# Kernel optimization log

Hardware: AMD Instinct MI355X
Metric: run time of the kernel (lower is better)

Reference implementation:

```python
import jax, jax.numpy as jnp
import numpy as np

B, T, DIM, H, HD = 1, 4096, 1024, 8, 128
ATTN_SCALE = 0.12


def _rms_norm(x):
    # F.rms_norm with default eps = finfo(dtype).eps, no learned weight
    eps = jnp.asarray(jnp.finfo(x.dtype).eps, x.dtype)
    return x * jax.lax.rsqrt(jnp.mean(x * x, axis=-1, keepdims=True) + eps)


def _rotary(x):
    # x: [B, T, H, D]; half-rotary: last D/2 freqs are zero (identity)
    t, d = x.shape[1], x.shape[-1]
    freqs = (1.0 / 1024.0) ** jnp.linspace(0.0, 1.0, d // 4, dtype=jnp.float32)
    freqs = jnp.concatenate([freqs, jnp.zeros(d // 4, dtype=jnp.float32)])
    theta = jnp.arange(t, dtype=jnp.float32)[:, None] * freqs[None, :]  # [T, D/2]
    cos = jnp.cos(theta)[None, :, None, :]
    sin = jnp.sin(theta)[None, :, None, :]
    x1, x2 = jnp.split(x.astype(jnp.float32), 2, axis=-1)
    y = jnp.concatenate([x1 * cos + x2 * sin, -x1 * sin + x2 * cos], axis=-1)
    return y.astype(x.dtype)


def setup_inputs() -> dict:
    key = jax.random.key(0)
    k1, k2, k3, k4, k5 = jax.random.split(key, 5)
    std = 0.5 * DIM ** -0.5
    bound = (3.0 ** 0.5) * std
    x = jax.random.normal(k1, (B, T, DIM), dtype=jnp.float32)
    ve = jax.random.normal(k2, (B, T, DIM), dtype=jnp.float32)
    qkv_w = jax.random.uniform(k3, (3, H * HD, DIM), dtype=jnp.float32,
                               minval=-bound, maxval=bound)
    lambdas = jnp.array([0.5, 0.5], dtype=jnp.float32)
    # c_proj is zero-initialized in the source; use small random weights so the
    # output (and gradients) are non-trivial for correctness testing
    c_proj_w = jax.random.normal(k4, (DIM, H * HD), dtype=jnp.float32) * 0.02
    docs = jnp.sort(jax.random.randint(k5, (T,), 0, 8, dtype=jnp.int32))
    return {"x": x, "ve": ve, "qkv_w": qkv_w, "lambdas": lambdas,
            "c_proj_w": c_proj_w, "docs": docs}


def reference(x, ve, qkv_w, lambdas, c_proj_w, docs):
    b, t, _ = x.shape
    w = qkv_w.reshape(3 * H * HD, -1)              # [3*hdim, dim]
    qkv = (x @ w.T).reshape(b, t, 3, H, HD)        # chunk(3, dim=-2) == axis 2 here
    q, k, v = qkv[:, :, 0], qkv[:, :, 1], qkv[:, :, 2]
    q, k = _rms_norm(q), _rms_norm(k)
    q, k = _rotary(q), _rotary(k)
    v = lambdas[0] * v + lambdas[1] * ve.reshape(v.shape)
    # doc-causal mask: attend within the same document, causally
    i = jnp.arange(t)
    mask = (i[:, None] >= i[None, :]) & (docs[:, None] == docs[None, :])  # [T, T]
    scores = jnp.einsum('bihd,bjhd->bhij', q, k) * ATTN_SCALE
    scores = jnp.where(mask[None, None], scores, -jnp.inf)
    p = jax.nn.softmax(scores, axis=-1)
    y = jnp.einsum('bhij,bjhd->bihd', p, v).reshape(b, t, H * HD)
    return y @ c_proj_w.T
```

## Files before the change

### kernel.cpp

```cpp
#include <hip/hip_runtime.h>
#include <hip/hip_bf16.h>
#include <cstdint>

typedef __attribute__((ext_vector_type(8))) short sh8;
typedef __attribute__((ext_vector_type(4))) float f4;
typedef __attribute__((ext_vector_type(16))) float f16v;

#define T_SEQ 4096
#define DIMN  1024
#define NH    8
#define HDIM  128
#define NQKV  3072
#define ATTN_SCALE 0.12f

__device__ __forceinline__ ushort f2bf(float x) {
  __hip_bfloat16 b = __float2bfloat16(x);
  return *reinterpret_cast<ushort*>(&b);
}
__device__ __forceinline__ float bf2f(ushort u) {
  uint v = ((uint)u) << 16;
  float f;
  __builtin_memcpy(&f, &v, 4);
  return f;
}

#define GLDS16(g, l) \
  __builtin_amdgcn_global_load_lds((const __attribute__((address_space(1))) void*)(g), \
                                   (__attribute__((address_space(3))) void*)(l), 16, 0, 0)

template <int N>
__device__ __forceinline__ void wait_vmcnt() {
  if constexpr (N == 0)      asm volatile("s_waitcnt vmcnt(0)" ::: "memory");
  else if constexpr (N == 4) asm volatile("s_waitcnt vmcnt(4)" ::: "memory");
  else if constexpr (N == 6) asm volatile("s_waitcnt vmcnt(6)" ::: "memory");
  else if constexpr (N == 8) asm volatile("s_waitcnt vmcnt(8)" ::: "memory");
  __builtin_amdgcn_sched_barrier(0);
}
#define BAR __builtin_amdgcn_s_barrier()

__global__ __launch_bounds__(256) void k_prep(const float* __restrict__ x,
                                              const float* __restrict__ qw,
                                              const float* __restrict__ cw,
                                              ushort* __restrict__ xb, ushort* __restrict__ wb,
                                              ushort* __restrict__ cbuf,
                                              const int* __restrict__ docs, int* __restrict__ dstart) {
  const int b = blockIdx.x;
  if (b < 8192) {
    const int i = b * 256 + threadIdx.x;
    const float* src;
    ushort* dst;
    int j;
    if (i < 1048576)       { src = x;  dst = xb;   j = i; }
    else if (i < 1835008)  { src = qw; dst = wb;   j = i - 1048576; }
    else                   { src = cw; dst = cbuf; j = i - 1835008; }
    float4 v = reinterpret_cast<const float4*>(src)[j];
    ushort4 o;
    o.x = f2bf(v.x); o.y = f2bf(v.y); o.z = f2bf(v.z); o.w = f2bf(v.w);
    reinterpret_cast<ushort4*>(dst)[j] = o;
  } else {
    const int i = (b - 8192) * 256 + threadIdx.x;
    if (i < T_SEQ) {
      int d = docs[i];
      int lo = 0, hi = i;
      while (lo < hi) { int mid = (lo + hi) >> 1; if (docs[mid] < d) lo = mid + 1; else hi = mid; }
      dstart[i] = lo;
    }
  }
}

__global__ __launch_bounds__(512, 2) void k_gemm32(const ushort* __restrict__ A,
                                                   const ushort* __restrict__ B,
                                                   ushort* __restrict__ C,
                                                   int N, int K) {
  __shared__ ushort lds[2][512 * 64];
  const int tid = threadIdx.x;
  const int lane = tid & 63;
  const int w = tid >> 6;
  const int l5 = lane >> 5;
  const int lr32 = lane & 31;
  const int wave_m = w >> 2, wave_n = w & 3;

  const int bid = blockIdx.x;
  const int s = (bid & 7) * 32 + (bid >> 3);
  const int m0 = ((s >> 5) * 4 + ((s >> 3) & 3)) * 128;
  const int n0 = (s & 7) * 384;

  f16v acc[2][3];
#pragma unroll
  for (int i = 0; i < 2; ++i)
#pragma unroll
    for (int j = 0; j < 3; ++j)
#pragma unroll
      for (int r = 0; r < 16; ++r) acc[i][j][r] = 0.f;

  const int NT = K >> 6;

  auto STAGE4 = [&](int buf, int t, int ug) {
    const int k0 = t << 6;
#pragma unroll
    for (int uu = 0; uu < 4; ++uu) {
      const int u = ug * 4 + uu;
      const int row = u * 64 + (tid >> 3);
      const int c = (tid & 7) ^ (row & 7);
      const ushort* src = (u < 2) ? (A + (size_t)(m0 + row) * K + k0 + c * 8)
                                  : (B + (size_t)(n0 + row - 128) * K + k0 + c * 8);
      GLDS16(src, (char*)&lds[buf][0] + u * 8192 + w * 1024);
    }
  };

  STAGE4(0, 0, 0); STAGE4(0, 0, 1);
  wait_vmcnt<0>();
  BAR;

  int cur = 0;
  for (int t = 0; t < NT; ++t) {
    const bool more = (t + 1) < NT;
    const char* bb = (const char*)&lds[cur][0];

#define RD_FRAGS(ks, a, b)                                                        \
    _Pragma("unroll") for (int mt = 0; mt < 2; ++mt) {                            \
      const int row = wave_m * 64 + mt * 32 + lr32;                               \
      a[mt] = *(const sh8*)(bb + row * 128 + ((((ks) * 2 + l5) ^ (row & 7)) * 16));\
    }                                                                             \
    _Pragma("unroll") for (int nt = 0; nt < 3; ++nt) {                            \
      const int row = 128 + wave_n * 96 + nt * 32 + lr32;                         \
      b[nt] = *(const sh8*)(bb + row * 128 + ((((ks) * 2 + l5) ^ (row & 7)) * 16));\
    }

#define MFMA6(a, b)                                                               \
    __builtin_amdgcn_s_setprio(1);                                                \
    _Pragma("unroll") for (int mt = 0; mt < 2; ++mt)                              \
    _Pragma("unroll") for (int nt = 0; nt < 3; ++nt)                              \
      acc[mt][nt] = __builtin_amdgcn_mfma_f32_32x32x16_bf16(a[mt], b[nt],         \
                                                            acc[mt][nt], 0, 0, 0);\
    __builtin_amdgcn_s_setprio(0);

    {
      sh8 a[2], b[3];
      RD_FRAGS(0, a, b)
      if (more) STAGE4(cur ^ 1, t + 1, 0);
      MFMA6(a, b)
    }
    {
      sh8 a[2], b[3];
      RD_FRAGS(1, a, b)
      if (more) STAGE4(cur ^ 1, t + 1, 1);
      MFMA6(a, b)
    }
    BAR;
    {
      sh8 a[2], b[3];
      RD_FRAGS(2, a, b)
      MFMA6(a, b)
    }
    if (more) wait_vmcnt<4>();
    {
      sh8 a[2], b[3];
      RD_FRAGS(3, a, b)
      MFMA6(a, b)
    }
    if (more) wait_vmcnt<0>();
    BAR;
    cur ^= 1;
  }
#undef RD_FRAGS
#undef MFMA6

#pragma unroll
  for (int mt = 0; mt < 2; ++mt)
#pragma unroll
    for (int nt = 0; nt < 3; ++nt) {
      const int gcol = n0 + wave_n * 96 + nt * 32 + lr32;
#pragma unroll
      for (int r = 0; r < 16; ++r) {
        const int grow = m0 + wave_m * 64 + mt * 32 + (r & 3) + 8 * (r >> 2) + 4 * l5;
        C[(size_t)grow * N + gcol] = f2bf(acc[mt][nt][r]);
      }
    }
}

__global__ __launch_bounds__(256) void k_gemm2(const ushort* __restrict__ A,
                                               const ushort* __restrict__ B,
                                               float* __restrict__ C,
                                               int N, int K, int gx) {
  constexpr int BM = 128, BN = 128;
  constexpr int CHA = BM * 4;
  constexpr int CHT = (BM + BN) * 4;
  constexpr int LPW = CHT / 256;
  constexpr int TILEB = (BM + BN) * 64;

  __shared__ __attribute__((aligned(16))) char lds[3 * TILEB];

  const int tid = threadIdx.x;
  const int lane = tid & 63;
  const int w = tid >> 6;
  const int l5 = lane >> 5;
  const int lr32 = lane & 31;
  const int wm = w >> 1, wn = w & 1;

  const int nwg = gridDim.x;
  const int nb = (blockIdx.x & 7) * (nwg >> 3) + (blockIdx.x >> 3);
  const int m0 = (nb / gx) * BM;
  const int n0 = (nb % gx) * BN;

  f16v acc[2][2];
#pragma unroll
  for (int i = 0; i < 2; ++i)
#pragma unroll
    for (int j = 0; j < 2; ++j)
#pragma unroll
      for (int r = 0; r < 16; ++r) acc[i][j][r] = 0.f;

  const int NT = K >> 5;

  auto STAGE = [&](int t, int buf) {
    const int k0 = t << 5;
#pragma unroll
    for (int l = 0; l < LPW; ++l) {
      const int cb = (l * 4 + w) * 64;
      const int ch = cb + lane;
      const ushort* src;
      if (ch < CHA) {
        const int row = ch >> 2;
        const int cs = (ch & 3) ^ ((row >> 1) & 3);
        src = A + (size_t)(m0 + row) * K + k0 + cs * 8;
      } else {
        const int c2 = ch - CHA;
        const int row = c2 >> 2;
        const int cs = (c2 & 3) ^ ((row >> 1) & 3);
        src = B + (size_t)(n0 + row) * K + k0 + cs * 8;
      }
      GLDS16(src, lds + buf * TILEB + cb * 16);
    }
  };

  STAGE(0, 0);
  STAGE(1, 1);
  wait_vmcnt<LPW>();
  BAR;

  int bufc = 0;
  for (int t = 0; t < NT; ++t) {
    const bool more = (t + 2) < NT;
    if (more) STAGE(t + 2, bufc == 0 ? 2 : (bufc == 1 ? 0 : 1));

    const char* bb = lds + bufc * TILEB;
#pragma unroll
    for (int ks = 0; ks < 2; ++ks) {
      sh8 a[2], b[2];
#pragma unroll
      for (int mt = 0; mt < 2; ++mt) {
        const int row = wm * 64 + mt * 32 + lr32;
        a[mt] = *(const sh8*)(bb + row * 64 + (((ks * 2 + l5) ^ ((row >> 1) & 3)) * 16));
      }
#pragma unroll
      for (int nt = 0; nt < 2; ++nt) {
        const int row = wn * 64 + nt * 32 + lr32;
        b[nt] = *(const sh8*)(bb + BM * 64 + row * 64 + (((ks * 2 + l5) ^ ((row >> 1) & 3)) * 16));
      }
      __builtin_amdgcn_s_setprio(1);
#pragma unroll
      for (int mt = 0; mt < 2; ++mt)
#pragma unroll
        for (int nt = 0; nt < 2; ++nt)
          acc[mt][nt] = __builtin_amdgcn_mfma_f32_32x32x16_bf16(a[mt], b[nt], acc[mt][nt], 0, 0, 0);
      __builtin_amdgcn_s_setprio(0);
    }

    if (more) wait_vmcnt<LPW>();
    else      wait_vmcnt<0>();
    BAR;
    bufc = bufc == 2 ? 0 : bufc + 1;
  }

#pragma unroll
  for (int mt = 0; mt < 2; ++mt)
#pragma unroll
    for (int nt = 0; nt < 2; ++nt) {
      const int gcol = n0 + wn * 64 + nt * 32 + lr32;
#pragma unroll
      for (int r = 0; r < 16; ++r) {
        const int grow = m0 + wm * 64 + mt * 32 + (r & 3) + 8 * (r >> 2) + 4 * l5;
        C[(size_t)grow * N + gcol] = acc[mt][nt][r];
      }
    }
}

__global__ __launch_bounds__(256) void k_fuse(const ushort* __restrict__ qkvb,
                                              const float* __restrict__ ve,
                                              const float* __restrict__ lam,
                                              ushort* __restrict__ qh, ushort* __restrict__ kh,
                                              ushort* __restrict__ vh) {
  const int pair = blockIdx.x * 4 + (threadIdx.x >> 6);
  const int t = pair >> 3, h = pair & 7;
  const int l = threadIdx.x & 63;
  const ushort* base = qkvb + (size_t)t * NQKV + h * HDIM + 2 * l;
  uint qu = *reinterpret_cast<const uint*>(base);
  uint ku = *reinterpret_cast<const uint*>(base + 1024);
  uint vu = *reinterpret_cast<const uint*>(base + 2048);
  float q0 = bf2f((ushort)qu), q1 = bf2f((ushort)(qu >> 16));
  float k0 = bf2f((ushort)ku), k1 = bf2f((ushort)(ku >> 16));
  float v0 = bf2f((ushort)vu), v1 = bf2f((ushort)(vu >> 16));
  float sq = q0 * q0 + q1 * q1, sk = k0 * k0 + k1 * k1;
#pragma unroll
  for (int m = 1; m < 64; m <<= 1) { sq += __shfl_xor(sq, m); sk += __shfl_xor(sk, m); }
  const float eps = 1.1920928955078125e-07f;
  float rq = rsqrtf(sq * (1.f / 128.f) + eps);
  float rk = rsqrtf(sk * (1.f / 128.f) + eps);
  q0 *= rq; q1 *= rq; k0 *= rk; k1 *= rk;
  float c0 = 1.f, s0 = 0.f, c1 = 1.f, s1 = 0.f;
  if ((l & 31) < 16) {
    const int f0 = 2 * (l & 31);
    float fr0 = exp2f(-10.f * (float)f0 * (1.f / 31.f));
    float fr1 = exp2f(-10.f * (float)(f0 + 1) * (1.f / 31.f));
    sincosf((float)t * fr0, &s0, &c0);
    sincosf((float)t * fr1, &s1, &c1);
  }
  float qx0 = __shfl_xor(q0, 32), qx1 = __shfl_xor(q1, 32);
  float kx0 = __shfl_xor(k0, 32), kx1 = __shfl_xor(k1, 32);
  const float sgn = (l < 32) ? 1.f : -1.f;
  float qr0 = q0 * c0 + sgn * qx0 * s0;
  float qr1 = q1 * c1 + sgn * qx1 * s1;
  float kr0 = k0 * c0 + sgn * kx0 * s0;
  float kr1 = k1 * c1 + sgn * kx1 * s1;
  const float l0 = lam[0], l1 = lam[1];
  float2 vev = *reinterpret_cast<const float2*>(ve + (size_t)t * DIMN + h * HDIM + 2 * l);
  float vr0 = l0 * v0 + l1 * vev.x;
  float vr1 = l0 * v1 + l1 * vev.y;
  const size_t o = ((size_t)h * T_SEQ + t) * HDIM + 2 * l;
  *reinterpret_cast<uint*>(qh + o) = (uint)f2bf(qr0) | ((uint)f2bf(qr1) << 16);
  *reinterpret_cast<uint*>(kh + o) = (uint)f2bf(kr0) | ((uint)f2bf(kr1) << 16);
  *reinterpret_cast<uint*>(vh + o) = (uint)f2bf(vr0) | ((uint)f2bf(vr1) << 16);
}

__global__ __launch_bounds__(256) void k_vt(const ushort* __restrict__ vh, ushort* __restrict__ vt) {
  const int tb = blockIdx.x, db = blockIdx.y, h = blockIdx.z;
  __shared__ ushort L[64][68];
  const int tid = threadIdx.x;
  const int t0 = tb * 64, d0 = db * 64;
  const size_t ib = ((size_t)h * T_SEQ + t0) * HDIM + d0;
#pragma unroll
  for (int p = 0; p < 4; ++p) {
    const int row = p * 16 + (tid >> 4);
    const int c4 = (tid & 15) * 4;
    ushort4 v = *reinterpret_cast<const ushort4*>(vh + ib + (size_t)row * HDIM + c4);
    *reinterpret_cast<ushort4*>(&L[row][c4]) = v;
  }
  __syncthreads();
  const size_t ob = ((size_t)h * HDIM + d0) * T_SEQ + t0;
#pragma unroll
  for (int p = 0; p < 4; ++p) {
    const int drow = p * 16 + (tid >> 4);
    const int t4 = (tid & 15) * 4;
    ushort4 v;
    v.x = L[t4 + 0][drow]; v.y = L[t4 + 1][drow];
    v.z = L[t4 + 2][drow]; v.w = L[t4 + 3][drow];
    *reinterpret_cast<ushort4*>(vt + ob + (size_t)drow * T_SEQ + t4) = v;
  }
}

__global__ __launch_bounds__(256) void k_attn(const ushort* __restrict__ qh,
                                              const ushort* __restrict__ kh,
                                              const ushort* __restrict__ vt,
                                              const int* __restrict__ doc_start,
                                              ushort* __restrict__ y) {
  const int h  = blockIdx.x;
  const int qb = blockIdx.y;
  const int q0 = qb * 64;
  const int tid  = threadIdx.x;
  const int wave = tid >> 6;
  const int lane = tid & 63;
  const int lr = lane & 15, lg = lane >> 4;

  __shared__ ushort Ks[2][64 * 128];
  __shared__ ushort Vs[2][128 * 64];
  __shared__ ushort Ps[4][16 * 64];

  const ushort* Kg = kh + (size_t)h * T_SEQ * HDIM;
  const ushort* Vg = vt + (size_t)h * HDIM * T_SEQ;

  const int i_me = q0 + wave * 16 + lr;
  sh8 qf[4];
  {
    const ushort* qp = qh + ((size_t)h * T_SEQ + i_me) * HDIM + lg * 8;
#pragma unroll
    for (int c = 0; c < 4; ++c) qf[c] = *reinterpret_cast<const sh8*>(qp + c * 32);
  }
  const int ds_me = doc_start[i_me];
  const int ds_hi = doc_start[q0 + 63];
  const int kb0   = doc_start[q0] >> 6;

  const f4 fzero = {0.f, 0.f, 0.f, 0.f};
  f4 o_acc[8];
#pragma unroll
  for (int i = 0; i < 8; ++i) o_acc[i] = fzero;
  float m_me = -1e30f, l_me = 0.f;

  auto STAGE = [&](int b, int k0) {
#pragma unroll
    for (int p = 0; p < 4; ++p) {
      const int c = p * 256 + tid;
      const int row = c >> 4, cc = c & 15;
      GLDS16(Kg + (size_t)(k0 + row) * HDIM + (cc ^ (row & 7)) * 8,
             &Ks[b][(p * 256 + wave * 64) * 8]);
    }
#pragma unroll
    for (int p = 0; p < 4; ++p) {
      const int c = p * 256 + tid;
      const int d = c >> 3, cc = c & 7;
      GLDS16(Vg + (size_t)d * T_SEQ + k0 + (cc ^ (d & 7)) * 8,
             &Vs[b][(p * 256 + wave * 64) * 8]);
    }
  };

  int cur = 0;
  STAGE(0, kb0 * 64);

  const int sw = (lr & 7) << 4;

  for (int kb = kb0; kb <= qb; ++kb) {
    const int k0 = kb * 64;
    __syncthreads();
    if (kb < qb) STAGE(cur ^ 1, k0 + 64);

    const char* Kb = (const char*)&Ks[cur][0];
    const char* Vb = (const char*)&Vs[cur][0];
    char* Pw = (char*)&Ps[wave][0];

    f4 sacc[4];
#pragma unroll
    for (int jt = 0; jt < 4; ++jt) sacc[jt] = fzero;
#pragma unroll
    for (int jt = 0; jt < 4; ++jt)
#pragma unroll
      for (int c = 0; c < 4; ++c) {
        sh8 kf = *reinterpret_cast<const sh8*>(Kb + (jt * 16 + lr) * 256 + ((c * 64 + lg * 16) ^ sw));
        sacc[jt] = __builtin_amdgcn_mfma_f32_16x16x32_bf16(kf, qf[c], sacc[jt], 0, 0, 0);
      }

    const bool fullblk = (kb < qb) && (ds_hi <= k0);
    float p[4][4];
#pragma unroll
    for (int jt = 0; jt < 4; ++jt)
#pragma unroll
      for (int r = 0; r < 4; ++r) {
        float s = sacc[jt][r] * ATTN_SCALE;
        const int j = k0 + jt * 16 + lg * 4 + r;
        bool valid = fullblk || ((j <= i_me) && (j >= ds_me));
        p[jt][r] = valid ? s : -1e30f;
      }
    float tm = -1e30f;
#pragma unroll
    for (int jt = 0; jt < 4; ++jt) {
      float a = fmaxf(p[jt][0], p[jt][1]), b = fmaxf(p[jt][2], p[jt][3]);
      tm = fmaxf(tm, fmaxf(a, b));
    }
    tm = fmaxf(tm, __shfl_xor(tm, 16));
    tm = fmaxf(tm, __shfl_xor(tm, 32));
    const float mnew = fmaxf(m_me, tm);
    const float sc = __expf(m_me - mnew);
    m_me = mnew;
    float rs = 0.f;
#pragma unroll
    for (int jt = 0; jt < 4; ++jt)
#pragma unroll
      for (int r = 0; r < 4; ++r) {
        float pv = __expf(p[jt][r] - mnew);
        p[jt][r] = pv;
        rs += pv;
      }
    rs += __shfl_xor(rs, 16);
    rs += __shfl_xor(rs, 32);
    l_me = l_me * sc + rs;

#pragma unroll
    for (int jt = 0; jt < 4; ++jt) {
      uint2 u;
      u.x = (uint)f2bf(p[jt][0]) | ((uint)f2bf(p[jt][1]) << 16);
      u.y = (uint)f2bf(p[jt][2]) | ((uint)f2bf(p[jt][3]) << 16);
      *reinterpret_cast<uint2*>(Pw + lr * 128 + ((jt * 32 + lg * 8) ^ sw)) = u;
    }

    float sco[4];
#pragma unroll
    for (int rr = 0; rr < 4; ++rr) sco[rr] = __shfl(sc, lg * 4 + rr);
#pragma unroll
    for (int dt = 0; dt < 8; ++dt)
#pragma unroll
      for (int rr = 0; rr < 4; ++rr) o_acc[dt][rr] *= sco[rr];

#pragma unroll
    for (int ks = 0; ks < 2; ++ks) {
      sh8 pa = *reinterpret_cast<const sh8*>(Pw + lr * 128 + ((ks * 64 + lg * 16) ^ sw));
#pragma unroll
      for (int dt = 0; dt < 8; ++dt) {
        sh8 vf = *reinterpret_cast<const sh8*>(Vb + (dt * 16 + lr) * 128 + ((ks * 64 + lg * 16) ^ sw));
        o_acc[dt] = __builtin_amdgcn_mfma_f32_16x16x32_bf16(pa, vf, o_acc[dt], 0, 0, 0);
      }
    }

    __builtin_amdgcn_s_barrier();
    cur ^= 1;
  }

  float lo[4];
#pragma unroll
  for (int rr = 0; rr < 4; ++rr) lo[rr] = __shfl(l_me, lg * 4 + rr);
#pragma unroll
  for (int dt = 0; dt < 8; ++dt)
#pragma unroll
    for (int rr = 0; rr < 4; ++rr) {
      const int trow = q0 + wave * 16 + lg * 4 + rr;
      y[(size_t)trow * DIMN + h * HDIM + dt * 16 + lr] = f2bf(o_acc[dt][rr] / lo[rr]);
    }
}

extern "C" void kernel_launch(void* const* d_in, const int* in_sizes, int n_in,
                              void* d_out, int out_size, void* d_ws, size_t ws_size,
                              hipStream_t stream) {
  const float* x    = (const float*)d_in[0];
  const float* ve   = (const float*)d_in[1];
  const float* qkvw = (const float*)d_in[2];
  const float* lam  = (const float*)d_in[3];
  const float* cpw  = (const float*)d_in[4];
  const int*   docs = (const int*)d_in[5];
  float* out = (float*)d_out;
  char* ws = (char*)d_ws;

  ushort* qkvb = (ushort*)(ws);
  ushort* xb   = (ushort*)(ws + (24ull << 20));
  ushort* wb   = (ushort*)(ws + (32ull << 20));
  ushort* cb   = (ushort*)(ws + (38ull << 20));
  ushort* qh   = (ushort*)(ws + (40ull << 20));
  ushort* kh   = (ushort*)(ws + (48ull << 20));
  ushort* vh   = (ushort*)(ws + (56ull << 20));
  ushort* vt   = (ushort*)(ws + (64ull << 20));
  ushort* yb   = (ushort*)(ws + (72ull << 20));
  int*  dstart = (int*)(ws + (80ull << 20));

  k_prep<<<8192 + 16, 256, 0, stream>>>(x, qkvw, cpw, xb, wb, cb, docs, dstart);

  k_gemm32<<<256, 512, 0, stream>>>(xb, wb, qkvb, NQKV, DIMN);

  k_fuse<<<T_SEQ * NH / 4, 256, 0, stream>>>(qkvb, ve, lam, qh, kh, vh);
  k_vt<<<dim3(T_SEQ / 64, HDIM / 64, NH), 256, 0, stream>>>(vh, vt);

  k_attn<<<dim3(NH, T_SEQ / 64), 256, 0, stream>>>(qh, kh, vt, dstart, yb);

  k_gemm2<<<256, 256, 0, stream>>>(yb, cb, out, DIMN, DIMN, DIMN / 128);
}
```

Before: 102.5 us.

## Fuse V transpose into QKV epilogue kernel and retile QKV GEMM to 256x256

Merges the norm/rotary/value-mix kernel with the separate V transpose kernel. V is staged in shared memory and written directly in transposed layout, which removes the intermediate vh buffer round trip and one launch. The QKV GEMM moves from 128x384 tiles on 256 blocks to 256x256 tiles on 192 blocks, with 4x2 MFMA fragments per wave and a mid-iteration vmcnt wait removed. Output stores in both GEMMs become nontemporal. The new GEMM grid leaves some CUs idle, and the fused kernel processes 16 tokens per wave sequentially, which may reduce parallelism.

```diff
diff --git a/kernel.cpp b/kernel.cpp
--- a/kernel.cpp
+++ b/kernel.cpp
@@ -32,7 +32,6 @@
 __device__ __forceinline__ void wait_vmcnt() {
   if constexpr (N == 0)      asm volatile("s_waitcnt vmcnt(0)" ::: "memory");
   else if constexpr (N == 4) asm volatile("s_waitcnt vmcnt(4)" ::: "memory");
-  else if constexpr (N == 6) asm volatile("s_waitcnt vmcnt(6)" ::: "memory");
   else if constexpr (N == 8) asm volatile("s_waitcnt vmcnt(8)" ::: "memory");
   __builtin_amdgcn_sched_barrier(0);
 }
@@ -68,10 +67,10 @@
   }
 }
 
-__global__ __launch_bounds__(512, 2) void k_gemm32(const ushort* __restrict__ A,
-                                                   const ushort* __restrict__ B,
-                                                   ushort* __restrict__ C,
-                                                   int N, int K) {
+__global__ __launch_bounds__(512, 2) void k_gemm256(const ushort* __restrict__ A,
+                                                    const ushort* __restrict__ B,
+                                                    ushort* __restrict__ C,
+                                                    int N, int K) {
   __shared__ ushort lds[2][512 * 64];
   const int tid = threadIdx.x;
   const int lane = tid & 63;
@@ -80,16 +79,15 @@
   const int lr32 = lane & 31;
   const int wave_m = w >> 2, wave_n = w & 3;
 
-  const int bid = blockIdx.x;
-  const int s = (bid & 7) * 32 + (bid >> 3);
-  const int m0 = ((s >> 5) * 4 + ((s >> 3) & 3)) * 128;
-  const int n0 = (s & 7) * 384;
-
-  f16v acc[2][3];
-#pragma unroll
-  for (int i = 0; i < 2; ++i)
-#pragma unroll
-    for (int j = 0; j < 3; ++j)
+  const int nb = (blockIdx.x & 7) * 24 + (blockIdx.x >> 3);
+  const int m0 = (nb / 12) * 256;
+  const int n0 = (nb % 12) * 256;
+
+  f16v acc[4][2];
+#pragma unroll
+  for (int i = 0; i < 4; ++i)
+#pragma unroll
+    for (int j = 0; j < 2; ++j)
 #pragma unroll
       for (int r = 0; r < 16; ++r) acc[i][j][r] = 0.f;
 
@@ -102,8 +100,8 @@
       const int u = ug * 4 + uu;
       const int row = u * 64 + (tid >> 3);
       const int c = (tid & 7) ^ (row & 7);
-      const ushort* src = (u < 2) ? (A + (size_t)(m0 + row) * K + k0 + c * 8)
-                                  : (B + (size_t)(n0 + row - 128) * K + k0 + c * 8);
+      const ushort* src = (row < 256 ? A + (size_t)(m0 + row) * K
+                                     : B + (size_t)(n0 + row - 256) * K) + k0 + c * 8;
       GLDS16(src, (char*)&lds[buf][0] + u * 8192 + w * 1024);
     }
   };
@@ -117,64 +115,63 @@
     const bool more = (t + 1) < NT;
     const char* bb = (const char*)&lds[cur][0];
 
-#define RD_FRAGS(ks, a, b)                                                        \
-    _Pragma("unroll") for (int mt = 0; mt < 2; ++mt) {                            \
-      const int row = wave_m * 64 + mt * 32 + lr32;                               \
+#define RD6(ks, a, b)                                                              \
+    _Pragma("unroll") for (int mt = 0; mt < 4; ++mt) {                             \
+      const int row = wave_m * 128 + mt * 32 + lr32;                               \
       a[mt] = *(const sh8*)(bb + row * 128 + ((((ks) * 2 + l5) ^ (row & 7)) * 16));\
-    }                                                                             \
-    _Pragma("unroll") for (int nt = 0; nt < 3; ++nt) {                            \
-      const int row = 128 + wave_n * 96 + nt * 32 + lr32;                         \
+    }                                                                              \
+    _Pragma("unroll") for (int nt = 0; nt < 2; ++nt) {                             \
+      const int row = 256 + wave_n * 64 + nt * 32 + lr32;                          \
       b[nt] = *(const sh8*)(bb + row * 128 + ((((ks) * 2 + l5) ^ (row & 7)) * 16));\
     }
 
-#define MFMA6(a, b)                                                               \
-    __builtin_amdgcn_s_setprio(1);                                                \
-    _Pragma("unroll") for (int mt = 0; mt < 2; ++mt)                              \
-    _Pragma("unroll") for (int nt = 0; nt < 3; ++nt)                              \
-      acc[mt][nt] = __builtin_amdgcn_mfma_f32_32x32x16_bf16(a[mt], b[nt],         \
-                                                            acc[mt][nt], 0, 0, 0);\
+#define MFMA8(a, b)                                                                \
+    __builtin_amdgcn_s_setprio(1);                                                 \
+    _Pragma("unroll") for (int mt = 0; mt < 4; ++mt)                               \
+    _Pragma("unroll") for (int nt = 0; nt < 2; ++nt)                               \
+      acc[mt][nt] = __builtin_amdgcn_mfma_f32_32x32x16_bf16(a[mt], b[nt],          \
+                                                            acc[mt][nt], 0, 0, 0); \
     __builtin_amdgcn_s_setprio(0);
 
     {
-      sh8 a[2], b[3];
-      RD_FRAGS(0, a, b)
+      sh8 a[4], b[2];
+      RD6(0, a, b)
       if (more) STAGE4(cur ^ 1, t + 1, 0);
-      MFMA6(a, b)
+      MFMA8(a, b)
     }
     {
-      sh8 a[2], b[3];
-      RD_FRAGS(1, a, b)
+      sh8 a[4], b[2];
+      RD6(1, a, b)
       if (more) STAGE4(cur ^ 1, t + 1, 1);
-      MFMA6(a, b)
+      MFMA8(a, b)
     }
     BAR;
     {
-      sh8 a[2], b[3];
-      RD_FRAGS(2, a, b)
-      MFMA6(a, b)
-    }
-    if (more) wait_vmcnt<4>();
+      sh8 a[4], b[2];
+      RD6(2, a, b)
+      MFMA8(a, b)
+    }
     {
-      sh8 a[2], b[3];
-      RD_FRAGS(3, a, b)
-      MFMA6(a, b)
+      sh8 a[4], b[2];
+      RD6(3, a, b)
+      MFMA8(a, b)
     }
     if (more) wait_vmcnt<0>();
     BAR;
     cur ^= 1;
   }
-#undef RD_FRAGS
-#undef MFMA6
-
-#pragma unroll
-  for (int mt = 0; mt < 2; ++mt)
-#pragma unroll
-    for (int nt = 0; nt < 3; ++nt) {
-      const int gcol = n0 + wave_n * 96 + nt * 32 + lr32;
+#undef RD6
+#undef MFMA8
+
+#pragma unroll
+  for (int mt = 0; mt < 4; ++mt)
+#pragma unroll
+    for (int nt = 0; nt < 2; ++nt) {
+      const int gcol = n0 + wave_n * 64 + nt * 32 + lr32;
 #pragma unroll
       for (int r = 0; r < 16; ++r) {
-        const int grow = m0 + wave_m * 64 + mt * 32 + (r & 3) + 8 * (r >> 2) + 4 * l5;
-        C[(size_t)grow * N + gcol] = f2bf(acc[mt][nt][r]);
+        const int grow = m0 + wave_m * 128 + mt * 32 + (r & 3) + 8 * (r >> 2) + 4 * l5;
+        __builtin_nontemporal_store(f2bf(acc[mt][nt][r]), &C[(size_t)grow * N + gcol]);
       }
     }
 }
@@ -185,8 +182,6 @@
                                                int N, int K, int gx) {
   constexpr int BM = 128, BN = 128;
   constexpr int CHA = BM * 4;
-  constexpr int CHT = (BM + BN) * 4;
-  constexpr int LPW = CHT / 256;
   constexpr int TILEB = (BM + BN) * 64;
 
   __shared__ __attribute__((aligned(16))) char lds[3 * TILEB];
@@ -216,7 +211,7 @@
   auto STAGE = [&](int t, int buf) {
     const int k0 = t << 5;
 #pragma unroll
-    for (int l = 0; l < LPW; ++l) {
+    for (int l = 0; l < 4; ++l) {
       const int cb = (l * 4 + w) * 64;
       const int ch = cb + lane;
       const ushort* src;
@@ -236,7 +231,7 @@
 
   STAGE(0, 0);
   STAGE(1, 1);
-  wait_vmcnt<LPW>();
+  wait_vmcnt<4>();
   BAR;
 
   int bufc = 0;
@@ -267,7 +262,7 @@
       __builtin_amdgcn_s_setprio(0);
     }
 
-    if (more) wait_vmcnt<LPW>();
+    if (more) wait_vmcnt<4>();
     else      wait_vmcnt<0>();
     BAR;
     bufc = bufc == 2 ? 0 : bufc + 1;
@@ -281,81 +276,80 @@
 #pragma unroll
       for (int r = 0; r < 16; ++r) {
         const int grow = m0 + wm * 64 + mt * 32 + (r & 3) + 8 * (r >> 2) + 4 * l5;
-        C[(size_t)grow * N + gcol] = acc[mt][nt][r];
-      }
-    }
-}
-
-__global__ __launch_bounds__(256) void k_fuse(const ushort* __restrict__ qkvb,
-                                              const float* __restrict__ ve,
-                                              const float* __restrict__ lam,
-                                              ushort* __restrict__ qh, ushort* __restrict__ kh,
-                                              ushort* __restrict__ vh) {
-  const int pair = blockIdx.x * 4 + (threadIdx.x >> 6);
-  const int t = pair >> 3, h = pair & 7;
+        __builtin_nontemporal_store(acc[mt][nt][r], &C[(size_t)grow * N + gcol]);
+      }
+    }
+}
+
+__global__ __launch_bounds__(256) void k_fuse2(const ushort* __restrict__ qkvb,
+                                               const float* __restrict__ ve,
+                                               const float* __restrict__ lam,
+                                               ushort* __restrict__ qh, ushort* __restrict__ kh,
+                                               ushort* __restrict__ vt) {
+  const int h  = blockIdx.x & 7;
+  const int t0 = (blockIdx.x >> 3) * 64;
+  const int w = threadIdx.x >> 6;
   const int l = threadIdx.x & 63;
-  const ushort* base = qkvb + (size_t)t * NQKV + h * HDIM + 2 * l;
-  uint qu = *reinterpret_cast<const uint*>(base);
-  uint ku = *reinterpret_cast<const uint*>(base + 1024);
-  uint vu = *reinterpret_cast<const uint*>(base + 2048);
-  float q0 = bf2f((ushort)qu), q1 = bf2f((ushort)(qu >> 16));
-  float k0 = bf2f((ushort)ku), k1 = bf2f((ushort)(ku >> 16));
-  float v0 = bf2f((ushort)vu), v1 = bf2f((ushort)(vu >> 16));
-  float sq = q0 * q0 + q1 * q1, sk = k0 * k0 + k1 * k1;
-#pragma unroll
-  for (int m = 1; m < 64; m <<= 1) { sq += __shfl_xor(sq, m); sk += __shfl_xor(sk, m); }
+  __shared__ ushort VL[64][130];
+
+  const float l0 = lam[0], l1 = lam[1];
   const float eps = 1.1920928955078125e-07f;
-  float rq = rsqrtf(sq * (1.f / 128.f) + eps);
-  float rk = rsqrtf(sk * (1.f / 128.f) + eps);
-  q0 *= rq; q1 *= rq; k0 *= rk; k1 *= rk;
-  float c0 = 1.f, s0 = 0.f, c1 = 1.f, s1 = 0.f;
-  if ((l & 31) < 16) {
+
+  float fr0 = 0.f, fr1 = 0.f;
+  const bool rot = (l & 31) < 16;
+  if (rot) {
     const int f0 = 2 * (l & 31);
-    float fr0 = exp2f(-10.f * (float)f0 * (1.f / 31.f));
-    float fr1 = exp2f(-10.f * (float)(f0 + 1) * (1.f / 31.f));
-    sincosf((float)t * fr0, &s0, &c0);
-    sincosf((float)t * fr1, &s1, &c1);
-  }
-  float qx0 = __shfl_xor(q0, 32), qx1 = __shfl_xor(q1, 32);
-  float kx0 = __shfl_xor(k0, 32), kx1 = __shfl_xor(k1, 32);
+    fr0 = exp2f(-10.f * (float)f0 * (1.f / 31.f));
+    fr1 = exp2f(-10.f * (float)(f0 + 1) * (1.f / 31.f));
+  }
   const float sgn = (l < 32) ? 1.f : -1.f;
-  float qr0 = q0 * c0 + sgn * qx0 * s0;
-  float qr1 = q1 * c1 + sgn * qx1 * s1;
-  float kr0 = k0 * c0 + sgn * kx0 * s0;
-  float kr1 = k1 * c1 + sgn * kx1 * s1;
-  const float l0 = lam[0], l1 = lam[1];
-  float2 vev = *reinterpret_cast<const float2*>(ve + (size_t)t * DIMN + h * HDIM + 2 * l);
-  float vr0 = l0 * v0 + l1 * vev.x;
-  float vr1 = l0 * v1 + l1 * vev.y;
-  const size_t o = ((size_t)h * T_SEQ + t) * HDIM + 2 * l;
-  *reinterpret_cast<uint*>(qh + o) = (uint)f2bf(qr0) | ((uint)f2bf(qr1) << 16);
-  *reinterpret_cast<uint*>(kh + o) = (uint)f2bf(kr0) | ((uint)f2bf(kr1) << 16);
-  *reinterpret_cast<uint*>(vh + o) = (uint)f2bf(vr0) | ((uint)f2bf(vr1) << 16);
-}
-
-__global__ __launch_bounds__(256) void k_vt(const ushort* __restrict__ vh, ushort* __restrict__ vt) {
-  const int tb = blockIdx.x, db = blockIdx.y, h = blockIdx.z;
-  __shared__ ushort L[64][68];
-  const int tid = threadIdx.x;
-  const int t0 = tb * 64, d0 = db * 64;
-  const size_t ib = ((size_t)h * T_SEQ + t0) * HDIM + d0;
-#pragma unroll
-  for (int p = 0; p < 4; ++p) {
-    const int row = p * 16 + (tid >> 4);
-    const int c4 = (tid & 15) * 4;
-    ushort4 v = *reinterpret_cast<const ushort4*>(vh + ib + (size_t)row * HDIM + c4);
-    *reinterpret_cast<ushort4*>(&L[row][c4]) = v;
+
+  for (int i = 0; i < 16; ++i) {
+    const int lt = i * 4 + w;
+    const int t = t0 + lt;
+    const ushort* base = qkvb + (size_t)t * NQKV + h * HDIM + 2 * l;
+    uint qu = *reinterpret_cast<const uint*>(base);
+    uint ku = *reinterpret_cast<const uint*>(base + 1024);
+    uint vu = *reinterpret_cast<const uint*>(base + 2048);
+    float q0 = bf2f((ushort)qu), q1 = bf2f((ushort)(qu >> 16));
+    float k0 = bf2f((ushort)ku), k1 = bf2f((ushort)(ku >> 16));
+    float v0 = bf2f((ushort)vu), v1 = bf2f((ushort)(vu >> 16));
+    float sq = q0 * q0 + q1 * q1, sk = k0 * k0 + k1 * k1;
+#pragma unroll
+    for (int m = 1; m < 64; m <<= 1) { sq += __shfl_xor(sq, m); sk += __shfl_xor(sk, m); }
+    float rq = rsqrtf(sq * (1.f / 128.f) + eps);
+    float rk = rsqrtf(sk * (1.f / 128.f) + eps);
+    q0 *= rq; q1 *= rq; k0 *= rk; k1 *= rk;
+    float c0 = 1.f, s0 = 0.f, c1 = 1.f, s1 = 0.f;
+    if (rot) {
+      sincosf((float)t * fr0, &s0, &c0);
+      sincosf((float)t * fr1, &s1, &c1);
+    }
+    float qx0 = __shfl_xor(q0, 32), qx1 = __shfl_xor(q1, 32);
+    float kx0 = __shfl_xor(k0, 32), kx1 = __shfl_xor(k1, 32);
+    float qr0 = q0 * c0 + sgn * qx0 * s0;
+    float qr1 = q1 * c1 + sgn * qx1 * s1;
+    float kr0 = k0 * c0 + sgn * kx0 * s0;
+    float kr1 = k1 * c1 + sgn * kx1 * s1;
+    float2 vev = *reinterpret_cast<const float2*>(ve + (size_t)t * DIMN + h * HDIM + 2 * l);
+    float vr0 = l0 * v0 + l1 * vev.x;
+    float vr1 = l0 * v1 + l1 * vev.y;
+    const size_t o = ((size_t)h * T_SEQ + t) * HDIM + 2 * l;
+    *reinterpret_cast<uint*>(qh + o) = (uint)f2bf(qr0) | ((uint)f2bf(qr1) << 16);
+    *reinterpret_cast<uint*>(kh + o) = (uint)f2bf(kr0) | ((uint)f2bf(kr1) << 16);
+    *reinterpret_cast<uint*>(&VL[lt][2 * l]) = (uint)f2bf(vr0) | ((uint)f2bf(vr1) << 16);
   }
   __syncthreads();
-  const size_t ob = ((size_t)h * HDIM + d0) * T_SEQ + t0;
-#pragma unroll
-  for (int p = 0; p < 4; ++p) {
-    const int drow = p * 16 + (tid >> 4);
-    const int t4 = (tid & 15) * 4;
-    ushort4 v;
-    v.x = L[t4 + 0][drow]; v.y = L[t4 + 1][drow];
-    v.z = L[t4 + 2][drow]; v.w = L[t4 + 3][drow];
-    *reinterpret_cast<ushort4*>(vt + ob + (size_t)drow * T_SEQ + t4) = v;
+
+  const int d = threadIdx.x >> 1;
+  const int th = (threadIdx.x & 1) * 32;
+  ushort* dst = vt + ((size_t)h * HDIM + d) * T_SEQ + t0 + th;
+#pragma unroll
+  for (int j0 = 0; j0 < 32; j0 += 8) {
+    sh8 v;
+#pragma unroll
+    for (int e = 0; e < 8; ++e) v[e] = (short)VL[th + j0 + e][d];
+    *reinterpret_cast<sh8*>(dst + j0) = v;
   }
 }
 
@@ -533,17 +527,15 @@
   ushort* cb   = (ushort*)(ws + (38ull << 20));
   ushort* qh   = (ushort*)(ws + (40ull << 20));
   ushort* kh   = (ushort*)(ws + (48ull << 20));
-  ushort* vh   = (ushort*)(ws + (56ull << 20));
   ushort* vt   = (ushort*)(ws + (64ull << 20));
   ushort* yb   = (ushort*)(ws + (72ull << 20));
   int*  dstart = (int*)(ws + (80ull << 20));
 
   k_prep<<<8192 + 16, 256, 0, stream>>>(x, qkvw, cpw, xb, wb, cb, docs, dstart);
 
-  k_gemm32<<<256, 512, 0, stream>>>(xb, wb, qkvb, NQKV, DIMN);
-
-  k_fuse<<<T_SEQ * NH / 4, 256, 0, stream>>>(qkvb, ve, lam, qh, kh, vh);
-  k_vt<<<dim3(T_SEQ / 64, HDIM / 64, NH), 256, 0, stream>>>(vh, vt);
+  k_gemm256<<<192, 512, 0, stream>>>(xb, wb, qkvb, NQKV, DIMN);
+
+  k_fuse2<<<T_SEQ / 64 * NH, 256, 0, stream>>>(qkvb, ve, lam, qh, kh, vt);
 
   k_attn<<<dim3(NH, T_SEQ / 64), 256, 0, stream>>>(qh, kh, vt, dstart, yb);
 
```

After: 111.9 us. +9.2%, slower.
